# Kernel optimization log

Measured on AMD Instinct MI355X. Metric: run time of the kernel, lower is better.

## Reference

```python
import jax, jax.numpy as jnp
import numpy as np

B, S, D, H = 2, 2048, 512, 8
HD = D // H
SPARSITY = 0.15
KTOP = max(1, int(S * SPARSITY))          # 307 important rows
HALF_WIN = min(32, S // 4) // 2           # 16 -> window |i-j| <= 16
RC = min(16, S // 8)                      # 16 random links per query token


def setup_inputs() -> dict:
    key = jax.random.key(0)
    ks = jax.random.split(key, 8)
    s = 0.02
    return {
        "x":  jax.random.normal(ks[0], (B, S, D), jnp.float32),
        "Wq": jax.random.normal(ks[1], (D, D), jnp.float32) * s,
        "bq": jnp.zeros((D,), jnp.float32),
        "Wk": jax.random.normal(ks[2], (D, D), jnp.float32) * s,
        "bk": jnp.zeros((D,), jnp.float32),
        "Wv": jax.random.normal(ks[3], (D, D), jnp.float32) * s,
        "bv": jnp.zeros((D,), jnp.float32),
        "Wo": jax.random.normal(ks[4], (D, D), jnp.float32) * s,
        "bo": jnp.zeros((D,), jnp.float32),
        "Ws1": jax.random.normal(ks[5], (D, D // 2), jnp.float32) * s,
        "bs1": jnp.zeros((D // 2,), jnp.float32),
        "Ws2": jax.random.normal(ks[6], (D // 2, 1), jnp.float32) * s,
        "bs2": jnp.zeros((1,), jnp.float32),
        # models torch.randperm(S)[:RC] per (b, i); duplicates are harmless for set-to-1
        "rand_idx": jax.random.randint(ks[7], (B, S, RC), 0, S, jnp.int32),
    }


def _sparse_mask(x, Ws1, bs1, Ws2, bs2, rand_idx):
    # importance scorer: Linear -> ReLU -> Linear -> Sigmoid, squeeze(-1)
    imp = jax.nn.sigmoid(jax.nn.relu(x @ Ws1 + bs1) @ Ws2 + bs2)[..., 0]  # [B,S]
    _, top_idx = jax.lax.top_k(imp, KTOP)                                  # [B,KTOP]
    brange = jnp.arange(B)
    row_imp = jnp.zeros((B, S), bool).at[brange[:, None], top_idx].set(True)
    idx = jnp.arange(S)
    win = jnp.abs(idx[:, None] - idx[None, :]) <= HALF_WIN                 # [S,S]
    rmask = jnp.zeros((B, S, S), bool).at[
        brange[:, None, None], idx[None, :, None], rand_idx].set(True)    # [B,S,S]
    mask = row_imp[:, :, None] | win[None, :, :] | rmask                   # [B,S,S]
    tril = idx[:, None] >= idx[None, :]                                    # causal (mask * (causal==0))
    return mask & tril


def reference(x, Wq, bq, Wk, bk, Wv, bv, Wo, bo, Ws1, bs1, Ws2, bs2, rand_idx):
    allowed = _sparse_mask(x, Ws1, bs1, Ws2, bs2, rand_idx)                # [B,S,S] bool
    q = (x @ Wq + bq).reshape(B, S, H, HD).transpose(0, 2, 1, 3)           # [B,H,S,HD]
    k = (x @ Wk + bk).reshape(B, S, H, HD).transpose(0, 2, 1, 3)
    v = (x @ Wv + bv).reshape(B, S, H, HD).transpose(0, 2, 1, 3)
    scores = jnp.einsum('bhid,bhjd->bhij', q, k) / jnp.sqrt(jnp.float32(HD))
    scores = jnp.where(allowed[:, None, :, :], scores, -jnp.inf)
    attn = jax.nn.softmax(scores, axis=-1)                                 # every row has j=i allowed
    out = jnp.einsum('bhij,bhjd->bhid', attn, v)
    out = out.transpose(0, 2, 1, 3).reshape(B, S, D)
    return out @ Wo + bo
```

## Files before the change

### kernel.cpp

```cpp
#include <hip/hip_runtime.h>
#include <math.h>

typedef unsigned short u16;
typedef unsigned int u32;
typedef unsigned long long u64;
typedef short bf16x8 __attribute__((ext_vector_type(8)));
typedef float f32x4 __attribute__((ext_vector_type(4)));

constexpr int NB = 2, NS = 2048, ND = 512, NH = 8, NHD = 64;
constexpr int NKTOP = 307, NHWIN = 16, NRC = 16;
constexpr int NILIST = 320;
constexpr int NSPAR = NS - NKTOP;
constexpr int NSPAD = 1744;
constexpr int NCHUNK = 4;
constexpr int LDSPAD = 40;

__device__ __forceinline__ u16 f2bf(float f) {
  u32 u = __builtin_bit_cast(u32, f);
  u32 r = (u + 0x7FFFu + ((u >> 16) & 1u)) >> 16;
  return (u16)r;
}
__device__ __forceinline__ float bf2f(short v) {
  return __builtin_bit_cast(float, (u32)(u16)v << 16);
}

__global__ __launch_bounds__(256) void csa_cvt_w(const float* __restrict__ W0, const float* __restrict__ W1,
                                                 const float* __restrict__ W2, const float* __restrict__ W3,
                                                 u16* __restrict__ wt) {
  __shared__ float tile[32][33];
  int w = blockIdx.z;
  const float* src = (w == 0) ? W0 : (w == 1) ? W1 : (w == 2) ? W2 : W3;
  int kb = blockIdx.x * 32, nb = blockIdx.y * 32;
  int tx = threadIdx.x & 31, ty = threadIdx.x >> 5;
  for (int i = ty; i < 32; i += 8) tile[i][tx] = src[(size_t)(kb + i) * ND + nb + tx];
  __syncthreads();
  u16* dst = wt + (size_t)w * ND * ND;
  for (int i = ty; i < 32; i += 8) dst[(size_t)(nb + i) * ND + kb + tx] = f2bf(tile[tx][i]);
}

__global__ __launch_bounds__(256) void csa_scorer(const float* __restrict__ x, const float* __restrict__ Ws1,
                                                  const float* __restrict__ bs1, const float* __restrict__ Ws2,
                                                  float* __restrict__ part) {
  __shared__ float As[32][33];
  __shared__ float Bs[32][68];
  const int tid = threadIdx.x;
  const int m0 = blockIdx.x * 32, n0 = blockIdx.y * 64;
  const int r2 = (tid >> 4) * 2;
  const int c4 = (tid & 15) * 4;
  float acc[2][4] = {};
  const int arow = tid & 31, aks = (tid >> 5) * 4;
  const int bk = tid >> 3, bc = (tid & 7) * 8;
  for (int k0 = 0; k0 < ND; k0 += 32) {
    __syncthreads();
    float4 av = *(const float4*)(&x[(size_t)(m0 + arow) * ND + k0 + aks]);
    As[aks + 0][arow] = av.x;
    As[aks + 1][arow] = av.y;
    As[aks + 2][arow] = av.z;
    As[aks + 3][arow] = av.w;
    *(float4*)(&Bs[bk][bc]) = *(const float4*)(&Ws1[(size_t)(k0 + bk) * 256 + n0 + bc]);
    *(float4*)(&Bs[bk][bc + 4]) = *(const float4*)(&Ws1[(size_t)(k0 + bk) * 256 + n0 + bc + 4]);
    __syncthreads();
    for (int k = 0; k < 32; k++) {
      float a0 = As[k][r2], a1 = As[k][r2 + 1];
      float4 b = *(const float4*)(&Bs[k][c4]);
      acc[0][0] += a0 * b.x; acc[0][1] += a0 * b.y; acc[0][2] += a0 * b.z; acc[0][3] += a0 * b.w;
      acc[1][0] += a1 * b.x; acc[1][1] += a1 * b.y; acc[1][2] += a1 * b.z; acc[1][3] += a1 * b.w;
    }
  }
  float4 w2 = *(const float4*)(&Ws2[n0 + c4]);
  float4 b1 = *(const float4*)(&bs1[n0 + c4]);
  float p0 = fmaxf(acc[0][0] + b1.x, 0.f) * w2.x + fmaxf(acc[0][1] + b1.y, 0.f) * w2.y +
             fmaxf(acc[0][2] + b1.z, 0.f) * w2.z + fmaxf(acc[0][3] + b1.w, 0.f) * w2.w;
  float p1 = fmaxf(acc[1][0] + b1.x, 0.f) * w2.x + fmaxf(acc[1][1] + b1.y, 0.f) * w2.y +
             fmaxf(acc[1][2] + b1.z, 0.f) * w2.z + fmaxf(acc[1][3] + b1.w, 0.f) * w2.w;
  for (int off = 1; off < 16; off <<= 1) {
    p0 += __shfl_xor(p0, off, 64);
    p1 += __shfl_xor(p1, off, 64);
  }
  if ((tid & 15) == 0) {
    part[(size_t)(m0 + r2) * 4 + blockIdx.y] = p0;
    part[(size_t)(m0 + r2 + 1) * 4 + blockIdx.y] = p1;
  }
}

__global__ __launch_bounds__(256) void csa_rank(const float* __restrict__ part, int* __restrict__ rowimp) {
  __shared__ float vals[NS];
  const int b = blockIdx.y;
  {
    int t8 = threadIdx.x * 8;
    for (int e = 0; e < 8; e++) {
      float4 pp = *(const float4*)(&part[(size_t)(b * NS + t8 + e) * 4]);
      vals[t8 + e] = (pp.x + pp.y) + (pp.z + pp.w);
    }
  }
  __syncthreads();
  const int wave = threadIdx.x >> 6, lane = threadIdx.x & 63;
  const int s0 = blockIdx.x * 8 + wave * 2;
  const int s1 = s0 + 1;
  const float v0 = vals[s0], v1 = vals[s1];
  int r0 = 0, r1 = 0;
  for (int t = lane; t < NS; t += 64) {
    float u = vals[t];
    r0 += (int)((u > v0) | ((u == v0) & (t < s0)));
    r1 += (int)((u > v1) | ((u == v1) & (t < s1)));
  }
  for (int off = 1; off < 64; off <<= 1) {
    r0 += __shfl_xor(r0, off, 64);
    r1 += __shfl_xor(r1, off, 64);
  }
  if (lane == 0) {
    rowimp[b * NS + s0] = (r0 < NKTOP) ? 1 : 0;
    rowimp[b * NS + s1] = (r1 < NKTOP) ? 1 : 0;
  }
}

__global__ __launch_bounds__(256) void csa_ilist(const int* __restrict__ rowimp, int* __restrict__ ilist,
                                                 int* __restrict__ nlist) {
  __shared__ int cs[256];
  int b = blockIdx.x, t = threadIdx.x;
  int flags[8], sum = 0;
  for (int k = 0; k < 8; k++) {
    flags[k] = rowimp[b * NS + t * 8 + k];
    sum += flags[k];
  }
  cs[t] = sum;
  __syncthreads();
  for (int off = 1; off < 256; off <<= 1) {
    int v = (t >= off) ? cs[t - off] : 0;
    __syncthreads();
    cs[t] += v;
    __syncthreads();
  }
  int pos = cs[t] - sum;
  for (int k = 0; k < 8; k++) {
    int r = t * 8 + k;
    if (flags[k]) ilist[b * NILIST + pos++] = r;
    else nlist[b * NSPAD + (r - pos)] = r;
  }
  if (t < NILIST - NKTOP) ilist[b * NILIST + NKTOP + t] = -1;
  if (t < NSPAD - NSPAR) nlist[b * NSPAD + NSPAR + t] = -1;
}

__global__ __launch_bounds__(256) void csa_gemm_qkv(const float* __restrict__ x, const u16* __restrict__ Bt,
                                                    const float* __restrict__ bq, const float* __restrict__ bk,
                                                    const float* __restrict__ bv, u16* __restrict__ qb,
                                                    u16* __restrict__ kb, u16* __restrict__ vtb,
                                                    u16* __restrict__ vb) {
  __shared__ __attribute__((aligned(16))) u16 As[128 * LDSPAD];
  __shared__ __attribute__((aligned(16))) u16 Bs[64 * LDSPAD];
  const int tid = threadIdx.x;
  const int wave = tid >> 6, lane = tid & 63;
  const int quad = lane >> 4, col = lane & 15;
  const int m0 = blockIdx.x * 128;
  const int n0 = blockIdx.y * 64;
  const f32x4 zf = {0.f, 0.f, 0.f, 0.f};
  f32x4 acc[2][4] = {{zf, zf, zf, zf}, {zf, zf, zf, zf}};
  const int sar = tid >> 1, sak = (tid & 1) * 16;
  const int sbr = tid >> 2, sbk = (tid & 3) * 8;
  for (int k0 = 0; k0 < ND; k0 += 32) {
    __syncthreads();
    {
      const float* xp = &x[(size_t)(m0 + sar) * ND + k0 + sak];
      float4 v0 = *(const float4*)(xp), v1 = *(const float4*)(xp + 4);
      float4 v2 = *(const float4*)(xp + 8), v3 = *(const float4*)(xp + 12);
      u32 w0 = (u32)f2bf(v0.x) | ((u32)f2bf(v0.y) << 16);
      u32 w1 = (u32)f2bf(v0.z) | ((u32)f2bf(v0.w) << 16);
      u32 w2 = (u32)f2bf(v1.x) | ((u32)f2bf(v1.y) << 16);
      u32 w3 = (u32)f2bf(v1.z) | ((u32)f2bf(v1.w) << 16);
      u32 w4 = (u32)f2bf(v2.x) | ((u32)f2bf(v2.y) << 16);
      u32 w5 = (u32)f2bf(v2.z) | ((u32)f2bf(v2.w) << 16);
      u32 w6 = (u32)f2bf(v3.x) | ((u32)f2bf(v3.y) << 16);
      u32 w7 = (u32)f2bf(v3.z) | ((u32)f2bf(v3.w) << 16);
      u32* ap = (u32*)&As[sar * LDSPAD + sak];
      ap[0] = w0; ap[1] = w1; ap[2] = w2; ap[3] = w3;
      ap[4] = w4; ap[5] = w5; ap[6] = w6; ap[7] = w7;
    }
    *(uint4*)(&Bs[sbr * LDSPAD + sbk]) = *(const uint4*)(&Bt[(size_t)(n0 + sbr) * ND + k0 + sbk]);
    __syncthreads();
    bf16x8 af0 = *(const bf16x8*)(&As[(wave * 32 + col) * LDSPAD + quad * 8]);
    bf16x8 af1 = *(const bf16x8*)(&As[(wave * 32 + 16 + col) * LDSPAD + quad * 8]);
    for (int c = 0; c < 4; c++) {
      bf16x8 bfr = *(const bf16x8*)(&Bs[(c * 16 + col) * LDSPAD + quad * 8]);
      acc[0][c] = __builtin_amdgcn_mfma_f32_16x16x32_bf16(af0, bfr, acc[0][c], 0, 0, 0);
      acc[1][c] = __builtin_amdgcn_mfma_f32_16x16x32_bf16(af1, bfr, acc[1][c], 0, 0, 0);
    }
  }
  const int w = n0 >> 9;
  const float* bias = (w == 0) ? bq : (w == 1) ? bk : bv;
  for (int c = 0; c < 4; c++) {
    const int ng = n0 + c * 16 + col;
    const int nn = ng & 511, hh = nn >> 6, hd = nn & 63;
    const float bvv = bias[nn];
    for (int r = 0; r < 2; r++) {
      for (int rr = 0; rr < 4; rr++) {
        const int m = m0 + wave * 32 + r * 16 + quad * 4 + rr;
        const int bb = m >> 11, s = m & (NS - 1);
        u16 v16 = f2bf(acc[r][c][rr] + bvv);
        if (w == 0) qb[((size_t)(bb * NH + hh) * NS + s) * NHD + hd] = v16;
        else if (w == 1) kb[((size_t)(bb * NH + hh) * NS + s) * NHD + hd] = v16;
        else {
          vtb[((size_t)(bb * NH + hh) * NHD + hd) * NS + s] = v16;
          vb[((size_t)(bb * NH + hh) * NS + s) * NHD + hd] = v16;
        }
      }
    }
  }
}

__global__ __launch_bounds__(256) void csa_gemm_out(const u16* __restrict__ A, const u16* __restrict__ Bt,
                                                    const float* __restrict__ bias, float* __restrict__ outp) {
  __shared__ __attribute__((aligned(16))) u16 As[64 * LDSPAD];
  __shared__ __attribute__((aligned(16))) u16 Bs[64 * LDSPAD];
  const int tid = threadIdx.x;
  const int wave = tid >> 6, lane = tid & 63;
  const int quad = lane >> 4, col = lane & 15;
  const int m0 = blockIdx.x * 64;
  const int n0 = blockIdx.y * 64;
  const f32x4 zf = {0.f, 0.f, 0.f, 0.f};
  f32x4 acc[4] = {zf, zf, zf, zf};
  const int lrow = tid >> 2, lk = (tid & 3) * 8;
  for (int k0 = 0; k0 < ND; k0 += 32) {
    __syncthreads();
    *(uint4*)(&As[lrow * LDSPAD + lk]) = *(const uint4*)(&A[(size_t)(m0 + lrow) * ND + k0 + lk]);
    *(uint4*)(&Bs[lrow * LDSPAD + lk]) = *(const uint4*)(&Bt[(size_t)(n0 + lrow) * ND + k0 + lk]);
    __syncthreads();
    bf16x8 af = *(const bf16x8*)(&As[(wave * 16 + col) * LDSPAD + quad * 8]);
    for (int nt = 0; nt < 4; nt++) {
      bf16x8 bfr = *(const bf16x8*)(&Bs[(nt * 16 + col) * LDSPAD + quad * 8]);
      acc[nt] = __builtin_amdgcn_mfma_f32_16x16x32_bf16(af, bfr, acc[nt], 0, 0, 0);
    }
  }
  for (int nt = 0; nt < 4; nt++) {
    const int n = n0 + nt * 16 + col;
    const float bvv = bias[n];
    for (int r = 0; r < 4; r++) {
      const int m = m0 + wave * 16 + quad * 4 + r;
      outp[(size_t)m * ND + n] = acc[nt][r] + bvv;
    }
  }
}

__global__ __launch_bounds__(64) void csa_attn_imp(const u16* __restrict__ qb, const u16* __restrict__ kb,
                                                   const u16* __restrict__ vtb, const int* __restrict__ ilist,
                                                   float* __restrict__ pbuf) {
  const int lane = threadIdx.x;
  const int quad = lane >> 4, col = lane & 15;
  const int qt = blockIdx.x;
  const int chunk = blockIdx.y;
  const int bh = blockIdx.z;
  const int b = bh >> 3, h = bh & 7;

  const int* il = ilist + b * NILIST;
  const u16* qptr = qb + (size_t)(b * NH + h) * NS * NHD;
  const u16* kptr = kb + (size_t)(b * NH + h) * NS * NHD;
  const u16* vptr = vtb + (size_t)(b * NH + h) * NHD * NS;

  const int iq = il[qt * 16 + col];
  const int qrow = (iq < 0) ? 0 : iq;
  bf16x8 qf0 = *(const bf16x8*)(qptr + qrow * NHD + quad * 8);
  bf16x8 qf1 = *(const bf16x8*)(qptr + qrow * NHD + 32 + quad * 8);

  const f32x4 zf = {0.f, 0.f, 0.f, 0.f};
  float m_r[4], l_r[4];
  f32x4 of[4];
  int irow[4];
  for (int r = 0; r < 4; r++) {
    m_r[r] = -INFINITY;
    l_r[r] = 0.f;
    irow[r] = il[qt * 16 + quad * 4 + r];
  }
  for (int n = 0; n < 4; n++) of[n] = zf;

  __shared__ __attribute__((aligned(16))) u16 Pl[16 * LDSPAD];

  const int max_i = il[(qt * 16 + 15 > NKTOP - 1) ? (NKTOP - 1) : (qt * 16 + 15)];
  const int ntiles = (max_i >> 5) + 1;
  for (int t = chunk; t < ntiles; t += NCHUNK) {
    const int j0 = t * 32;
    f32x4 c0 = zf, c1 = zf;
    {
      bf16x8 k00 = *(const bf16x8*)(kptr + (j0 + col) * NHD + quad * 8);
      bf16x8 k01 = *(const bf16x8*)(kptr + (j0 + col) * NHD + 32 + quad * 8);
      c0 = __builtin_amdgcn_mfma_f32_16x16x32_bf16(qf0, k00, c0, 0, 0, 0);
      c0 = __builtin_amdgcn_mfma_f32_16x16x32_bf16(qf1, k01, c0, 0, 0, 0);
      bf16x8 k10 = *(const bf16x8*)(kptr + (j0 + 16 + col) * NHD + quad * 8);
      bf16x8 k11 = *(const bf16x8*)(kptr + (j0 + 16 + col) * NHD + 32 + quad * 8);
      c1 = __builtin_amdgcn_mfma_f32_16x16x32_bf16(qf0, k10, c1, 0, 0, 0);
      c1 = __builtin_amdgcn_mfma_f32_16x16x32_bf16(qf1, k11, c1, 0, 0, 0);
    }
    const int j_0 = j0 + col, j_1 = j0 + 16 + col;
    float p0s[4], p1s[4], alpha[4];
    for (int r = 0; r < 4; r++) {
      const int i = irow[r];
      float s0 = (j_0 <= i) ? c0[r] * 0.125f : -INFINITY;
      float s1 = (j_1 <= i) ? c1[r] * 0.125f : -INFINITY;
      float vmax = fmaxf(s0, s1);
      for (int off = 1; off < 16; off <<= 1) vmax = fmaxf(vmax, __shfl_xor(vmax, off, 64));
      float newm = fmaxf(m_r[r], vmax);
      bool dead = (newm == -INFINITY);
      float a = dead ? 1.f : __expf(m_r[r] - newm);
      float p0 = dead ? 0.f : __expf(s0 - newm);
      float p1 = dead ? 0.f : __expf(s1 - newm);
      float psum = p0 + p1;
      for (int off = 1; off < 16; off <<= 1) psum += __shfl_xor(psum, off, 64);
      m_r[r] = newm;
      l_r[r] = l_r[r] * a + psum;
      alpha[r] = a;
      p0s[r] = p0;
      p1s[r] = p1;
    }
    for (int n = 0; n < 4; n++)
      for (int r = 0; r < 4; r++) of[n][r] *= alpha[r];
    __syncthreads();
    for (int r = 0; r < 4; r++) {
      Pl[(quad * 4 + r) * LDSPAD + col] = f2bf(p0s[r]);
      Pl[(quad * 4 + r) * LDSPAD + 16 + col] = f2bf(p1s[r]);
    }
    __syncthreads();
    bf16x8 pf = *(const bf16x8*)(&Pl[col * LDSPAD + quad * 8]);
    for (int vn = 0; vn < 4; vn++) {
      bf16x8 vf = *(const bf16x8*)(vptr + (size_t)(vn * 16 + col) * NS + j0 + quad * 8);
      of[vn] = __builtin_amdgcn_mfma_f32_16x16x32_bf16(pf, vf, of[vn], 0, 0, 0);
    }
  }
  float* pr = pbuf + ((size_t)(bh * NCHUNK + chunk) * NILIST + qt * 16) * 66;
  for (int r = 0; r < 4; r++) {
    const int row = quad * 4 + r;
    if (col == 0) {
      pr[row * 66 + 0] = m_r[r];
      pr[row * 66 + 1] = l_r[r];
    }
    for (int vn = 0; vn < 4; vn++)
      pr[row * 66 + 2 + vn * 16 + col] = of[vn][r];
  }
}

__global__ __launch_bounds__(64) void csa_merge(const float* __restrict__ pbuf, const int* __restrict__ ilist,
                                                u16* __restrict__ attnb) {
  const int kp = blockIdx.x, h = blockIdx.y, b = blockIdx.z;
  const int lane = threadIdx.x;
  const int z = b * NH + h;
  float mc[NCHUNK], lc[NCHUNK], mstar = -INFINITY;
  for (int c = 0; c < NCHUNK; c++) {
    const float* base = pbuf + ((size_t)(z * NCHUNK + c) * NILIST + kp) * 66;
    mc[c] = base[0];
    lc[c] = base[1];
    mstar = fmaxf(mstar, mc[c]);
  }
  float lsum = 0.f, osum = 0.f;
  for (int c = 0; c < NCHUNK; c++) {
    const float* base = pbuf + ((size_t)(z * NCHUNK + c) * NILIST + kp) * 66;
    float w = (mc[c] == -INFINITY) ? 0.f : __expf(mc[c] - mstar);
    lsum += w * lc[c];
    osum += w * base[2 + lane];
  }
  const int i = ilist[b * NILIST + kp];
  attnb[((size_t)(b * NS + i) * NH + h) * NHD + lane] = f2bf(osum / lsum);
}

__global__ __launch_bounds__(256) void csa_attn_sparse(const u16* __restrict__ qb, const u16* __restrict__ kb,
                                                       const u16* __restrict__ vb, const int* __restrict__ nlist,
                                                       const int* __restrict__ rand_idx, u16* __restrict__ attnb) {
  __shared__ __attribute__((aligned(16))) u16 ql[4][64];
  __shared__ float pl[4][33];
  __shared__ int jl[4][33];
  const int wave = threadIdx.x >> 6, lane = threadIdx.x & 63;
  const int slot = blockIdx.x * 4 + wave;
  const int h = blockIdx.y, b = blockIdx.z;
  const int i = nlist[b * NSPAD + slot];
  const int iv = (i < 0) ? 0 : i;

  const u16* qrow = qb + ((size_t)(b * NH + h) * NS + iv) * NHD;
  const u16* kbase = kb + (size_t)(b * NH + h) * NS * NHD;
  const u16* vbase = vb + (size_t)(b * NH + h) * NS * NHD;

  if (lane < 8) *(bf16x8*)(&ql[wave][lane * 8]) = *(const bf16x8*)(qrow + lane * 8);
  __syncthreads();

  float sd = bf2f((short)ql[wave][lane]) * bf2f((short)kbase[(size_t)iv * NHD + lane]);
  for (int off = 1; off < 64; off <<= 1) sd += __shfl_xor(sd, off, 64);
  sd *= 0.125f;

  const int c = lane >> 1, half = lane & 1;
  int j, valid;
  if (c < 16) {
    j = i - NHWIN + c;
    valid = (j >= 0);
  } else {
    const int* rr = rand_idx + ((size_t)b * NS + iv) * NRC;
    const int cr = c - 16;
    j = rr[cr];
    valid = (j <= i - NHWIN - 1);
    for (int cp = 0; cp < cr; cp++) valid &= (rr[cp] != j);
  }
  const int jr = valid ? j : 0;
  float s = 0.f;
  {
    const u16* krow = kbase + (size_t)jr * NHD + half * 32;
    for (int c8 = 0; c8 < 4; c8++) {
      bf16x8 kv = *(const bf16x8*)(krow + c8 * 8);
      bf16x8 qv = *(const bf16x8*)(&ql[wave][half * 32 + c8 * 8]);
      for (int e = 0; e < 8; e++) s += bf2f(qv[e]) * bf2f(kv[e]);
    }
  }
  s += __shfl_xor(s, 1, 64);
  s = valid ? s * 0.125f : -INFINITY;

  float smax = s;
  for (int off = 1; off < 64; off <<= 1) smax = fmaxf(smax, __shfl_xor(smax, off, 64));
  smax = fmaxf(smax, sd);
  float p = valid ? __expf(s - smax) : 0.f;
  float pd = __expf(sd - smax);
  float pm = (half == 0) ? p : 0.f;
  for (int off = 1; off < 64; off <<= 1) pm += __shfl_xor(pm, off, 64);
  const float lsum = pm + pd;

  if (half == 0) {
    pl[wave][c] = p;
    jl[wave][c] = jr;
  }
  if (lane == 0) {
    pl[wave][32] = pd;
    jl[wave][32] = iv;
  }
  __syncthreads();

  float o = 0.f;
  for (int jj = 0; jj < 33; jj++) {
    const int jk = __builtin_amdgcn_readfirstlane(jl[wave][jj]);
    const float pj = pl[wave][jj];
    o += pj * bf2f((short)vbase[(size_t)jk * NHD + lane]);
  }
  if (i >= 0)
    attnb[((size_t)(b * NS + i) * NH + h) * NHD + lane] = f2bf(o / lsum);
}

extern "C" void kernel_launch(void* const* d_in, const int* in_sizes, int n_in,
                              void* d_out, int out_size, void* d_ws, size_t ws_size,
                              hipStream_t stream) {
  const float* x = (const float*)d_in[0];
  const float* bq = (const float*)d_in[2];
  const float* bk = (const float*)d_in[4];
  const float* bv = (const float*)d_in[6];
  const float* bo = (const float*)d_in[8];
  const float* Ws1 = (const float*)d_in[9];
  const float* bs1 = (const float*)d_in[10];
  const float* Ws2 = (const float*)d_in[11];
  const int* rand_idx = (const int*)d_in[13];
  float* out = (float*)d_out;

  char* p = (char*)d_ws;
  u16* wt = (u16*)p;         p += (size_t)4 * ND * ND * 2;
  u16* qbuf = (u16*)p;       p += (size_t)NB * NH * NS * NHD * 2;
  u16* kbuf = (u16*)p;       p += (size_t)NB * NH * NS * NHD * 2;
  u16* vtbuf = (u16*)p;      p += (size_t)NB * NH * NHD * NS * 2;
  u16* vbuf = (u16*)p;       p += (size_t)NB * NH * NS * NHD * 2;
  u16* attnb = (u16*)p;      p += (size_t)NB * NS * ND * 2;
  float* part = (float*)p;   p += (size_t)NB * NS * 4 * 4;
  int* rowimp = (int*)p;     p += (size_t)NB * NS * 4;
  int* ilist = (int*)p;      p += (size_t)NB * NILIST * 4;
  int* nlist = (int*)p;      p += (size_t)NB * NSPAD * 4;
  float* pbuf = (float*)p;

  csa_cvt_w<<<dim3(16, 16, 4), 256, 0, stream>>>((const float*)d_in[1], (const float*)d_in[3],
                                                 (const float*)d_in[5], (const float*)d_in[7], wt);

  csa_scorer<<<dim3(NB * NS / 32, 4), 256, 0, stream>>>(x, Ws1, bs1, Ws2, part);
  csa_rank<<<dim3(NS / 8, NB), 256, 0, stream>>>(part, rowimp);
  csa_ilist<<<dim3(NB), 256, 0, stream>>>(rowimp, ilist, nlist);

  csa_gemm_qkv<<<dim3(32, 24), 256, 0, stream>>>(x, wt, bq, bk, bv, qbuf, kbuf, vtbuf, vbuf);

  csa_attn_imp<<<dim3(NILIST / 16, NCHUNK, NB * NH), 64, 0, stream>>>(qbuf, kbuf, vtbuf, ilist, pbuf);
  csa_attn_sparse<<<dim3(NSPAD / 4, NH, NB), 256, 0, stream>>>(qbuf, kbuf, vbuf, nlist, rand_idx, attnb);
  csa_merge<<<dim3(NKTOP, NH, NB), 64, 0, stream>>>(pbuf, ilist, attnb);

  csa_gemm_out<<<dim3(64, 8), 256, 0, stream>>>(attnb, wt + 3 * (size_t)ND * ND, bo, out);
}
```

Before: 213.1 us.

## Enlarge tiles across weight conversion, scorer, output GEMM and important-row attention

Weight conversion now handles 64-wide K tiles and writes bf16 pairs as packed 32-bit stores. The scorer GEMM moves to 64x64 block tiles with a 4x4 register microtile per thread. The output projection GEMM uses K=64 steps with two MFMAs per step, halving the number of barriers. Important-row attention now processes 64 keys per tile with four score MFMAs, and the key range is split into 8 chunks instead of 4. These changes trade more register and LDS use, plus a larger partial buffer to merge, for fewer loop iterations and synchronisations.

```diff
diff --git a/kernel.cpp b/kernel.cpp
--- a/kernel.cpp
+++ b/kernel.cpp
@@ -12,8 +12,10 @@
 constexpr int NILIST = 320;
 constexpr int NSPAR = NS - NKTOP;
 constexpr int NSPAD = 1744;
-constexpr int NCHUNK = 4;
+constexpr int NCHUNK = 8;
 constexpr int LDSPAD = 40;
+constexpr int LDSK64 = 72;
+constexpr int PSTR = 72;
 
 __device__ __forceinline__ u16 f2bf(float f) {
   u32 u = __builtin_bit_cast(u32, f);
@@ -27,59 +29,61 @@
 __global__ __launch_bounds__(256) void csa_cvt_w(const float* __restrict__ W0, const float* __restrict__ W1,
                                                  const float* __restrict__ W2, const float* __restrict__ W3,
                                                  u16* __restrict__ wt) {
-  __shared__ float tile[32][33];
+  __shared__ float tile[64][33];
   int w = blockIdx.z;
   const float* src = (w == 0) ? W0 : (w == 1) ? W1 : (w == 2) ? W2 : W3;
-  int kb = blockIdx.x * 32, nb = blockIdx.y * 32;
+  int kb = blockIdx.x * 64, nb = blockIdx.y * 32;
   int tx = threadIdx.x & 31, ty = threadIdx.x >> 5;
-  for (int i = ty; i < 32; i += 8) tile[i][tx] = src[(size_t)(kb + i) * ND + nb + tx];
+  for (int i = ty; i < 64; i += 8) tile[i][tx] = src[(size_t)(kb + i) * ND + nb + tx];
   __syncthreads();
   u16* dst = wt + (size_t)w * ND * ND;
-  for (int i = ty; i < 32; i += 8) dst[(size_t)(nb + i) * ND + kb + tx] = f2bf(tile[tx][i]);
+  for (int n = ty; n < 32; n += 8) {
+    u32 pk = (u32)f2bf(tile[2 * tx][n]) | ((u32)f2bf(tile[2 * tx + 1][n]) << 16);
+    *(u32*)(&dst[(size_t)(nb + n) * ND + kb + 2 * tx]) = pk;
+  }
 }
 
 __global__ __launch_bounds__(256) void csa_scorer(const float* __restrict__ x, const float* __restrict__ Ws1,
                                                   const float* __restrict__ bs1, const float* __restrict__ Ws2,
                                                   float* __restrict__ part) {
-  __shared__ float As[32][33];
+  __shared__ float As[32][68];
   __shared__ float Bs[32][68];
   const int tid = threadIdx.x;
-  const int m0 = blockIdx.x * 32, n0 = blockIdx.y * 64;
-  const int r2 = (tid >> 4) * 2;
-  const int c4 = (tid & 15) * 4;
-  float acc[2][4] = {};
-  const int arow = tid & 31, aks = (tid >> 5) * 4;
+  const int m0 = blockIdx.x * 64, n0 = blockIdx.y * 64;
+  const int ty = tid >> 4, tx = tid & 15;
+  float acc[4][4] = {};
+  const int arow = tid & 63, aks = (tid >> 6) * 8;
   const int bk = tid >> 3, bc = (tid & 7) * 8;
   for (int k0 = 0; k0 < ND; k0 += 32) {
     __syncthreads();
-    float4 av = *(const float4*)(&x[(size_t)(m0 + arow) * ND + k0 + aks]);
-    As[aks + 0][arow] = av.x;
-    As[aks + 1][arow] = av.y;
-    As[aks + 2][arow] = av.z;
-    As[aks + 3][arow] = av.w;
+    {
+      float4 a0 = *(const float4*)(&x[(size_t)(m0 + arow) * ND + k0 + aks]);
+      float4 a1 = *(const float4*)(&x[(size_t)(m0 + arow) * ND + k0 + aks + 4]);
+      As[aks + 0][arow] = a0.x; As[aks + 1][arow] = a0.y;
+      As[aks + 2][arow] = a0.z; As[aks + 3][arow] = a0.w;
+      As[aks + 4][arow] = a1.x; As[aks + 5][arow] = a1.y;
+      As[aks + 6][arow] = a1.z; As[aks + 7][arow] = a1.w;
+    }
     *(float4*)(&Bs[bk][bc]) = *(const float4*)(&Ws1[(size_t)(k0 + bk) * 256 + n0 + bc]);
     *(float4*)(&Bs[bk][bc + 4]) = *(const float4*)(&Ws1[(size_t)(k0 + bk) * 256 + n0 + bc + 4]);
     __syncthreads();
     for (int k = 0; k < 32; k++) {
-      float a0 = As[k][r2], a1 = As[k][r2 + 1];
-      float4 b = *(const float4*)(&Bs[k][c4]);
-      acc[0][0] += a0 * b.x; acc[0][1] += a0 * b.y; acc[0][2] += a0 * b.z; acc[0][3] += a0 * b.w;
-      acc[1][0] += a1 * b.x; acc[1][1] += a1 * b.y; acc[1][2] += a1 * b.z; acc[1][3] += a1 * b.w;
-    }
-  }
-  float4 w2 = *(const float4*)(&Ws2[n0 + c4]);
-  float4 b1 = *(const float4*)(&bs1[n0 + c4]);
-  float p0 = fmaxf(acc[0][0] + b1.x, 0.f) * w2.x + fmaxf(acc[0][1] + b1.y, 0.f) * w2.y +
-             fmaxf(acc[0][2] + b1.z, 0.f) * w2.z + fmaxf(acc[0][3] + b1.w, 0.f) * w2.w;
-  float p1 = fmaxf(acc[1][0] + b1.x, 0.f) * w2.x + fmaxf(acc[1][1] + b1.y, 0.f) * w2.y +
-             fmaxf(acc[1][2] + b1.z, 0.f) * w2.z + fmaxf(acc[1][3] + b1.w, 0.f) * w2.w;
-  for (int off = 1; off < 16; off <<= 1) {
-    p0 += __shfl_xor(p0, off, 64);
-    p1 += __shfl_xor(p1, off, 64);
-  }
-  if ((tid & 15) == 0) {
-    part[(size_t)(m0 + r2) * 4 + blockIdx.y] = p0;
-    part[(size_t)(m0 + r2 + 1) * 4 + blockIdx.y] = p1;
+      float4 av = *(const float4*)(&As[k][ty * 4]);
+      float4 bv = *(const float4*)(&Bs[k][tx * 4]);
+      float aa[4] = {av.x, av.y, av.z, av.w};
+      float bb[4] = {bv.x, bv.y, bv.z, bv.w};
+      for (int i = 0; i < 4; i++)
+        for (int j = 0; j < 4; j++)
+          acc[i][j] += aa[i] * bb[j];
+    }
+  }
+  float4 w2 = *(const float4*)(&Ws2[n0 + tx * 4]);
+  float4 b1 = *(const float4*)(&bs1[n0 + tx * 4]);
+  for (int i = 0; i < 4; i++) {
+    float p = fmaxf(acc[i][0] + b1.x, 0.f) * w2.x + fmaxf(acc[i][1] + b1.y, 0.f) * w2.y +
+              fmaxf(acc[i][2] + b1.z, 0.f) * w2.z + fmaxf(acc[i][3] + b1.w, 0.f) * w2.w;
+    for (int off = 1; off < 16; off <<= 1) p += __shfl_xor(p, off, 64);
+    if (tx == 0) part[(size_t)(m0 + ty * 4 + i) * 4 + blockIdx.y] = p;
   }
 }
 
@@ -209,8 +213,8 @@
 
 __global__ __launch_bounds__(256) void csa_gemm_out(const u16* __restrict__ A, const u16* __restrict__ Bt,
                                                     const float* __restrict__ bias, float* __restrict__ outp) {
-  __shared__ __attribute__((aligned(16))) u16 As[64 * LDSPAD];
-  __shared__ __attribute__((aligned(16))) u16 Bs[64 * LDSPAD];
+  __shared__ __attribute__((aligned(16))) u16 As[64 * LDSK64];
+  __shared__ __attribute__((aligned(16))) u16 Bs[64 * LDSK64];
   const int tid = threadIdx.x;
   const int wave = tid >> 6, lane = tid & 63;
   const int quad = lane >> 4, col = lane & 15;
@@ -218,16 +222,21 @@
   const int n0 = blockIdx.y * 64;
   const f32x4 zf = {0.f, 0.f, 0.f, 0.f};
   f32x4 acc[4] = {zf, zf, zf, zf};
-  const int lrow = tid >> 2, lk = (tid & 3) * 8;
-  for (int k0 = 0; k0 < ND; k0 += 32) {
-    __syncthreads();
-    *(uint4*)(&As[lrow * LDSPAD + lk]) = *(const uint4*)(&A[(size_t)(m0 + lrow) * ND + k0 + lk]);
-    *(uint4*)(&Bs[lrow * LDSPAD + lk]) = *(const uint4*)(&Bt[(size_t)(n0 + lrow) * ND + k0 + lk]);
-    __syncthreads();
-    bf16x8 af = *(const bf16x8*)(&As[(wave * 16 + col) * LDSPAD + quad * 8]);
+  const int sr = tid >> 2, sk = (tid & 3) * 16;
+  for (int k0 = 0; k0 < ND; k0 += 64) {
+    __syncthreads();
+    *(uint4*)(&As[sr * LDSK64 + sk]) = *(const uint4*)(&A[(size_t)(m0 + sr) * ND + k0 + sk]);
+    *(uint4*)(&As[sr * LDSK64 + sk + 8]) = *(const uint4*)(&A[(size_t)(m0 + sr) * ND + k0 + sk + 8]);
+    *(uint4*)(&Bs[sr * LDSK64 + sk]) = *(const uint4*)(&Bt[(size_t)(n0 + sr) * ND + k0 + sk]);
+    *(uint4*)(&Bs[sr * LDSK64 + sk + 8]) = *(const uint4*)(&Bt[(size_t)(n0 + sr) * ND + k0 + sk + 8]);
+    __syncthreads();
+    bf16x8 af0 = *(const bf16x8*)(&As[(wave * 16 + col) * LDSK64 + quad * 8]);
+    bf16x8 af1 = *(const bf16x8*)(&As[(wave * 16 + col) * LDSK64 + 32 + quad * 8]);
     for (int nt = 0; nt < 4; nt++) {
-      bf16x8 bfr = *(const bf16x8*)(&Bs[(nt * 16 + col) * LDSPAD + quad * 8]);
-      acc[nt] = __builtin_amdgcn_mfma_f32_16x16x32_bf16(af, bfr, acc[nt], 0, 0, 0);
+      bf16x8 bf0 = *(const bf16x8*)(&Bs[(nt * 16 + col) * LDSK64 + quad * 8]);
+      bf16x8 bf1 = *(const bf16x8*)(&Bs[(nt * 16 + col) * LDSK64 + 32 + quad * 8]);
+      acc[nt] = __builtin_amdgcn_mfma_f32_16x16x32_bf16(af0, bf0, acc[nt], 0, 0, 0);
+      acc[nt] = __builtin_amdgcn_mfma_f32_16x16x32_bf16(af1, bf1, acc[nt], 0, 0, 0);
     }
   }
   for (int nt = 0; nt < 4; nt++) {
@@ -271,56 +280,60 @@
   }
   for (int n = 0; n < 4; n++) of[n] = zf;
 
-  __shared__ __attribute__((aligned(16))) u16 Pl[16 * LDSPAD];
+  __shared__ __attribute__((aligned(16))) u16 Pl[16 * PSTR];
 
   const int max_i = il[(qt * 16 + 15 > NKTOP - 1) ? (NKTOP - 1) : (qt * 16 + 15)];
-  const int ntiles = (max_i >> 5) + 1;
+  const int ntiles = (max_i >> 6) + 1;
   for (int t = chunk; t < ntiles; t += NCHUNK) {
-    const int j0 = t * 32;
-    f32x4 c0 = zf, c1 = zf;
-    {
-      bf16x8 k00 = *(const bf16x8*)(kptr + (j0 + col) * NHD + quad * 8);
-      bf16x8 k01 = *(const bf16x8*)(kptr + (j0 + col) * NHD + 32 + quad * 8);
-      c0 = __builtin_amdgcn_mfma_f32_16x16x32_bf16(qf0, k00, c0, 0, 0, 0);
-      c0 = __builtin_amdgcn_mfma_f32_16x16x32_bf16(qf1, k01, c0, 0, 0, 0);
-      bf16x8 k10 = *(const bf16x8*)(kptr + (j0 + 16 + col) * NHD + quad * 8);
-      bf16x8 k11 = *(const bf16x8*)(kptr + (j0 + 16 + col) * NHD + 32 + quad * 8);
-      c1 = __builtin_amdgcn_mfma_f32_16x16x32_bf16(qf0, k10, c1, 0, 0, 0);
-      c1 = __builtin_amdgcn_mfma_f32_16x16x32_bf16(qf1, k11, c1, 0, 0, 0);
-    }
-    const int j_0 = j0 + col, j_1 = j0 + 16 + col;
-    float p0s[4], p1s[4], alpha[4];
+    const int j0 = t * 64;
+    f32x4 cg[4];
+    for (int g = 0; g < 4; g++) {
+      const int jb = j0 + g * 16;
+      bf16x8 k0f = *(const bf16x8*)(kptr + (jb + col) * NHD + quad * 8);
+      bf16x8 k1f = *(const bf16x8*)(kptr + (jb + col) * NHD + 32 + quad * 8);
+      f32x4 c = zf;
+      c = __builtin_amdgcn_mfma_f32_16x16x32_bf16(qf0, k0f, c, 0, 0, 0);
+      c = __builtin_amdgcn_mfma_f32_16x16x32_bf16(qf1, k1f, c, 0, 0, 0);
+      cg[g] = c;
+    }
+    float ps[4][4], alpha[4];
     for (int r = 0; r < 4; r++) {
       const int i = irow[r];
-      float s0 = (j_0 <= i) ? c0[r] * 0.125f : -INFINITY;
-      float s1 = (j_1 <= i) ? c1[r] * 0.125f : -INFINITY;
-      float vmax = fmaxf(s0, s1);
+      float s[4];
+      float vmax = -INFINITY;
+      for (int g = 0; g < 4; g++) {
+        s[g] = (j0 + g * 16 + col <= i) ? cg[g][r] * 0.125f : -INFINITY;
+        vmax = fmaxf(vmax, s[g]);
+      }
       for (int off = 1; off < 16; off <<= 1) vmax = fmaxf(vmax, __shfl_xor(vmax, off, 64));
       float newm = fmaxf(m_r[r], vmax);
       bool dead = (newm == -INFINITY);
       float a = dead ? 1.f : __expf(m_r[r] - newm);
-      float p0 = dead ? 0.f : __expf(s0 - newm);
-      float p1 = dead ? 0.f : __expf(s1 - newm);
-      float psum = p0 + p1;
+      float psum = 0.f;
+      for (int g = 0; g < 4; g++) {
+        float p = dead ? 0.f : __expf(s[g] - newm);
+        ps[r][g] = p;
+        psum += p;
+      }
       for (int off = 1; off < 16; off <<= 1) psum += __shfl_xor(psum, off, 64);
       m_r[r] = newm;
       l_r[r] = l_r[r] * a + psum;
       alpha[r] = a;
-      p0s[r] = p0;
-      p1s[r] = p1;
     }
     for (int n = 0; n < 4; n++)
       for (int r = 0; r < 4; r++) of[n][r] *= alpha[r];
     __syncthreads();
-    for (int r = 0; r < 4; r++) {
-      Pl[(quad * 4 + r) * LDSPAD + col] = f2bf(p0s[r]);
-      Pl[(quad * 4 + r) * LDSPAD + 16 + col] = f2bf(p1s[r]);
-    }
-    __syncthreads();
-    bf16x8 pf = *(const bf16x8*)(&Pl[col * LDSPAD + quad * 8]);
+    for (int r = 0; r < 4; r++)
+      for (int g = 0; g < 4; g++)
+        Pl[(quad * 4 + r) * PSTR + g * 16 + col] = f2bf(ps[r][g]);
+    __syncthreads();
+    bf16x8 pf0 = *(const bf16x8*)(&Pl[col * PSTR + quad * 8]);
+    bf16x8 pf1 = *(const bf16x8*)(&Pl[col * PSTR + 32 + quad * 8]);
     for (int vn = 0; vn < 4; vn++) {
-      bf16x8 vf = *(const bf16x8*)(vptr + (size_t)(vn * 16 + col) * NS + j0 + quad * 8);
-      of[vn] = __builtin_amdgcn_mfma_f32_16x16x32_bf16(pf, vf, of[vn], 0, 0, 0);
+      bf16x8 vf0 = *(const bf16x8*)(vptr + (size_t)(vn * 16 + col) * NS + j0 + quad * 8);
+      bf16x8 vf1 = *(const bf16x8*)(vptr + (size_t)(vn * 16 + col) * NS + j0 + 32 + quad * 8);
+      of[vn] = __builtin_amdgcn_mfma_f32_16x16x32_bf16(pf0, vf0, of[vn], 0, 0, 0);
+      of[vn] = __builtin_amdgcn_mfma_f32_16x16x32_bf16(pf1, vf1, of[vn], 0, 0, 0);
     }
   }
   float* pr = pbuf + ((size_t)(bh * NCHUNK + chunk) * NILIST + qt * 16) * 66;
@@ -462,10 +475,10 @@
   int* nlist = (int*)p;      p += (size_t)NB * NSPAD * 4;
   float* pbuf = (float*)p;
 
-  csa_cvt_w<<<dim3(16, 16, 4), 256, 0, stream>>>((const float*)d_in[1], (const float*)d_in[3],
-                                                 (const float*)d_in[5], (const float*)d_in[7], wt);
-
-  csa_scorer<<<dim3(NB * NS / 32, 4), 256, 0, stream>>>(x, Ws1, bs1, Ws2, part);
+  csa_cvt_w<<<dim3(8, 16, 4), 256, 0, stream>>>((const float*)d_in[1], (const float*)d_in[3],
+                                                (const float*)d_in[5], (const float*)d_in[7], wt);
+
+  csa_scorer<<<dim3(NB * NS / 64, 4), 256, 0, stream>>>(x, Ws1, bs1, Ws2, part);
   csa_rank<<<dim3(NS / 8, NB), 256, 0, stream>>>(part, rowimp);
   csa_ilist<<<dim3(NB), 256, 0, stream>>>(rowimp, ilist, nlist);
 
```

Result: no change. 209.5 us (-1.7%).
